# Kernel tuning notes

Hardware: AMD Instinct MI355X
Metric: run time of the kernel (lower is better)

## Reference

```python
import jax, jax.numpy as jnp
import numpy as np

HIDDEN = 2048
NUM_HEADS = 16
NUM_KV_HEADS = 4
HEAD_DIM = 128
ROPE_BASE = 10000.0


def apply_rope(x):
    # x: [B, H, S, D]; standard half-split RoPE
    B, H, S, D = x.shape
    half = D // 2
    inv_freq = 1.0 / (ROPE_BASE ** (jnp.arange(half, dtype=jnp.float32) / half))
    ang = jnp.arange(S, dtype=jnp.float32)[:, None] * inv_freq[None, :]  # [S, half]
    cos = jnp.cos(ang).astype(x.dtype)
    sin = jnp.sin(ang).astype(x.dtype)
    x1, x2 = x[..., :half], x[..., half:]
    return jnp.concatenate([x1 * cos - x2 * sin, x1 * sin + x2 * cos], axis=-1)


def setup_inputs() -> dict:
    key = jax.random.key(0)
    ks = jax.random.split(key, 6)
    B, S = 2, 2048
    sd = 1.0 / np.sqrt(HIDDEN)
    x = jax.random.normal(ks[0], (B, S, HIDDEN), dtype=jnp.float32)
    wq = jax.random.normal(ks[1], (NUM_HEADS * HEAD_DIM, HIDDEN), dtype=jnp.float32) * sd
    wk = jax.random.normal(ks[2], (NUM_KV_HEADS * HEAD_DIM, HIDDEN), dtype=jnp.float32) * sd
    wv = jax.random.normal(ks[3], (NUM_KV_HEADS * HEAD_DIM, HIDDEN), dtype=jnp.float32) * sd
    wo = jax.random.normal(ks[4], (HIDDEN, NUM_HEADS * HEAD_DIM), dtype=jnp.float32) * sd
    key_weights = jnp.ones((NUM_HEADS,), dtype=jnp.float32)
    return {"x": x, "wq": wq, "wk": wk, "wv": wv, "wo": wo, "key_weights": key_weights}


def reference(x, wq, wk, wv, wo, key_weights):
    B, S, _ = x.shape
    g = NUM_HEADS // NUM_KV_HEADS
    scale = HEAD_DIM ** -0.5
    # projections -> [B, H, S, D]
    q = (x @ wq.T).reshape(B, S, NUM_HEADS, HEAD_DIM).transpose(0, 2, 1, 3)
    k = (x @ wk.T).reshape(B, S, NUM_KV_HEADS, HEAD_DIM).transpose(0, 2, 1, 3)
    v = (x @ wv.T).reshape(B, S, NUM_KV_HEADS, HEAD_DIM).transpose(0, 2, 1, 3)
    q = apply_rope(q)
    k = apply_rope(k)
    # GQA expansion (repeat_interleave over head dim)
    k = jnp.repeat(k, g, axis=1)
    v = jnp.repeat(v, g, axis=1)
    # per-head key scaling fused into K
    k = k * key_weights[None, :, None, None]
    scores = jnp.einsum("bhqd,bhkd->bhqk", q, k) * scale
    causal = jnp.triu(jnp.ones((S, S), dtype=bool), k=1)
    scores = jnp.where(causal, -jnp.inf, scores)
    attn = jax.nn.softmax(scores, axis=-1)
    out = jnp.einsum("bhqk,bhkd->bhqd", attn, v)
    out = out.transpose(0, 2, 1, 3).reshape(B, S, NUM_HEADS * HEAD_DIM)
    return out @ wo.T
```

## Files before the change

kernel.cpp:

```cpp
#include <hip/hip_runtime.h>

#define S_LEN 2048
#define HID 2048
#define NH 16
#define HD 128
#define QKV_N 3072
#define KCOL 2048
#define VCOL 2560

typedef unsigned short ushort_t;
using bf16x8 = __attribute__((ext_vector_type(8))) __bf16;
using f32x4 = __attribute__((ext_vector_type(4))) float;
using ushort8 = __attribute__((ext_vector_type(8))) unsigned short;
using ushort4v = __attribute__((ext_vector_type(4))) unsigned short;

__device__ __forceinline__ unsigned short f2bf(float f) {
  unsigned int u = __float_as_uint(f);
  unsigned int r = u + 0x7FFFu + ((u >> 16) & 1u);
  return (unsigned short)(r >> 16);
}
__device__ __forceinline__ float bf2f(unsigned short h) {
  return __uint_as_float(((unsigned int)h) << 16);
}

__device__ __forceinline__ void gload_lds16(const ushort_t* g, ushort_t* lds) {
  __builtin_amdgcn_global_load_lds(
      (const __attribute__((address_space(1))) unsigned int*)g,
      (__attribute__((address_space(3))) unsigned int*)lds, 16, 0, 0);
}

__global__ void cast_bf16_kernel(const float* __restrict__ in, ushort_t* __restrict__ out, int n4) {
  int i = blockIdx.x * 256 + threadIdx.x;
  if (i >= n4) return;
  float4 v = reinterpret_cast<const float4*>(in)[i];
  ushort4v o;
  o.x = f2bf(v.x); o.y = f2bf(v.y); o.z = f2bf(v.z); o.w = f2bf(v.w);
  reinterpret_cast<ushort4v*>(out)[i] = o;
}

__global__ void rope_table_kernel(float* __restrict__ cosT, float* __restrict__ sinT) {
  int i = blockIdx.x * 256 + threadIdx.x;
  if (i >= S_LEN * 64) return;
  int s = i >> 6, j = i & 63;
  float inv = __expf(-(float)j * (9.210340371976184f / 64.0f));
  float ang = (float)s * inv;
  float sv, cv;
  sincosf(ang, &sv, &cv);
  cosT[i] = cv;
  sinT[i] = sv;
}

__global__ void rope_apply_kernel(ushort_t* __restrict__ base, const float* __restrict__ cosT,
                                  const float* __restrict__ sinT, const float* __restrict__ kw,
                                  int stride, int lognh, float scale, int useKw, int n) {
  int idx = blockIdx.x * 256 + threadIdx.x;
  if (idx >= n) return;
  int row = idx >> lognh;
  int p = idx & ((1 << lognh) - 1);
  int h = p >> 6, j = p & 63;
  int s = row & (S_LEN - 1);
  float c = cosT[(s << 6) + j];
  float sn = sinT[(s << 6) + j];
  long a = (long)row * stride + h * HD;
  float x1 = bf2f(base[a + j]);
  float x2 = bf2f(base[a + j + 64]);
  float wsc = useKw ? (scale * kw[h]) : scale;
  base[a + j] = f2bf((x1 * c - x2 * sn) * wsc);
  base[a + j + 64] = f2bf((x1 * sn + x2 * c) * wsc);
}

__global__ __launch_bounds__(256) void transpose_v_kernel(const ushort_t* __restrict__ qkv,
                                                          ushort_t* __restrict__ vt) {
  __shared__ ushort_t T[64][76];
  int bid = blockIdx.x;
  int dd = bid & 7;
  int tt = bid >> 3;
  int tid = threadIdx.x;
#pragma unroll
  for (int it = 0; it < 2; ++it) {
    int c = tid + it * 256;
    int i = c >> 3, j8 = c & 7;
    ushort8 v = *reinterpret_cast<const ushort8*>(
        qkv + (long)(tt * 64 + i) * QKV_N + VCOL + dd * 64 + j8 * 8);
    *reinterpret_cast<ushort8*>(&T[i][j8 * 8]) = v;
  }
  __syncthreads();
#pragma unroll
  for (int it = 0; it < 2; ++it) {
    int c = tid + it * 256;
    int jd = c >> 3, sc = c & 7;
    ushort8 o;
#pragma unroll
    for (int e = 0; e < 8; ++e) o[e] = T[sc * 8 + e][jd];
    int token = tt * 64 + sc * 8;
    int b = token >> 11, s = token & (S_LEN - 1);
    int vd = dd * 64 + jd;
    *reinterpret_cast<ushort8*>(vt + ((long)(b * 512 + vd) << 11) + s) = o;
  }
}

__device__ __forceinline__ void store_c(ushort_t* p, float v) { *p = f2bf(v); }
__device__ __forceinline__ void store_c(float* p, float v) { *p = v; }

template <typename OT>
__global__ __launch_bounds__(256) void gemm_bt_kernel(const ushort_t* __restrict__ A,
                                                      const ushort_t* __restrict__ W,
                                                      OT* __restrict__ C, int M, int N, int K) {
  __shared__ ushort_t As[128 * 32];
  __shared__ ushort_t Bs[128 * 32];
  const int tid = threadIdx.x;
  const int l = tid & 63, w = tid >> 6;
  const int wr = w >> 1, wc = w & 1;
  const int r = l & 15, g = l >> 4;
  const long arow0 = (long)blockIdx.y * 128;
  const long brow0 = (long)blockIdx.x * 128;

  f32x4 acc[4][4] = {};

  const int c0 = tid, c1 = tid + 256;
  const ushort_t* a_src0 = A + (arow0 + (c0 >> 2)) * K + ((c0 & 3) << 3);
  const ushort_t* a_src1 = A + (arow0 + (c1 >> 2)) * K + ((c1 & 3) << 3);
  const ushort_t* b_src0 = W + (brow0 + (c0 >> 2)) * K + ((c0 & 3) << 3);
  const ushort_t* b_src1 = W + (brow0 + (c1 >> 2)) * K + ((c1 & 3) << 3);
  ushort_t* a_dst0 = &As[c0 * 8];
  ushort_t* a_dst1 = &As[c1 * 8];
  ushort_t* b_dst0 = &Bs[c0 * 8];
  ushort_t* b_dst1 = &Bs[c1 * 8];

  for (int kk = 0; kk < K; kk += 32) {
    gload_lds16(a_src0 + kk, a_dst0);
    gload_lds16(a_src1 + kk, a_dst1);
    gload_lds16(b_src0 + kk, b_dst0);
    gload_lds16(b_src1 + kk, b_dst1);
    __syncthreads();
    bf16x8 af[4], bw[4];
#pragma unroll
    for (int mi = 0; mi < 4; ++mi)
      af[mi] = *reinterpret_cast<const bf16x8*>(&As[(wr * 64 + mi * 16 + r) * 32 + g * 8]);
#pragma unroll
    for (int ni = 0; ni < 4; ++ni)
      bw[ni] = *reinterpret_cast<const bf16x8*>(&Bs[(wc * 64 + ni * 16 + r) * 32 + g * 8]);
#pragma unroll
    for (int mi = 0; mi < 4; ++mi)
#pragma unroll
      for (int ni = 0; ni < 4; ++ni)
        acc[mi][ni] = __builtin_amdgcn_mfma_f32_16x16x32_bf16(af[mi], bw[ni], acc[mi][ni], 0, 0, 0);
    __syncthreads();
  }

#pragma unroll
  for (int mi = 0; mi < 4; ++mi)
#pragma unroll
    for (int ni = 0; ni < 4; ++ni) {
      int col = (int)brow0 + wc * 64 + ni * 16 + r;
#pragma unroll
      for (int j = 0; j < 4; ++j) {
        int row = (int)arow0 + wr * 64 + mi * 16 + g * 4 + j;
        store_c(&C[(long)row * N + col], acc[mi][ni][j]);
      }
    }
}

__global__ __launch_bounds__(256) void flash_attn_kernel(const ushort_t* __restrict__ qkv,
                                                         const ushort_t* __restrict__ Vt,
                                                         ushort_t* __restrict__ AO) {
  __shared__ ushort_t Ks[64 * 128];
  __shared__ ushort_t Vts[128 * 64];
  __shared__ ushort_t Ps[4][16 * 68];

  const int bid = blockIdx.x;
  const int pr = bid & 15;
  const int h = (bid >> 4) & 15;
  const int b = bid >> 8;
  const int tid = threadIdx.x;
  const int l = tid & 63, w = tid >> 6;
  const int r = l & 15, g = l >> 4;
  const int kvh = h >> 2;

  const ushort_t* Qb = qkv + (long)b * S_LEN * QKV_N + h * HD;
  const ushort_t* Kb = qkv + (long)b * S_LEN * QKV_N + KCOL + kvh * HD;
  const ushort_t* Vb = Vt + ((long)(b * 512 + kvh * HD) << 11);

  for (int pi = 0; pi < 2; ++pi) {
    const int qt = pi ? (31 - pr) : pr;
    const int qg = qt * 64 + w * 16;
    const long qrow0 = (long)b * S_LEN + qg;

    bf16x8 qa[4];
#pragma unroll
    for (int ks = 0; ks < 4; ++ks)
      qa[ks] = *reinterpret_cast<const bf16x8*>(Qb + (long)(qg + r) * QKV_N + ks * 32 + g * 8);

    f32x4 acc[8] = {};
    float mrow[4], lrow[4];
#pragma unroll
    for (int j = 0; j < 4; ++j) { mrow[j] = -1e30f; lrow[j] = 0.f; }

    for (int kv = 0; kv <= qt; ++kv) {
      __syncthreads();
#pragma unroll
      for (int i = 0; i < 4; ++i) {
        int c = tid + i * 256;
        int krow = c >> 4, cc = c & 15;
        int scc = cc ^ (krow & 7);
        gload_lds16(Kb + (long)(kv * 64 + krow) * QKV_N + scc * 8, &Ks[c * 8]);
      }
#pragma unroll
      for (int i = 0; i < 4; ++i) {
        int c = tid + i * 256;
        int vrow = c >> 3, cc = c & 7;
        int scc = cc ^ (vrow & 7);
        gload_lds16(Vb + ((long)vrow << 11) + kv * 64 + scc * 8, &Vts[c * 8]);
      }
      __syncthreads();

      f32x4 s[4] = {};
#pragma unroll
      for (int ks = 0; ks < 4; ++ks) {
        bf16x8 kf[4];
#pragma unroll
        for (int ni = 0; ni < 4; ++ni) {
          int n = ni * 16 + r;
          int chunk = (ks * 4 + g) ^ (n & 7);
          kf[ni] = *reinterpret_cast<const bf16x8*>(
              reinterpret_cast<const char*>(Ks) + n * 256 + chunk * 16);
        }
#pragma unroll
        for (int ni = 0; ni < 4; ++ni)
          s[ni] = __builtin_amdgcn_mfma_f32_16x16x32_bf16(qa[ks], kf[ni], s[ni], 0, 0, 0);
      }
      if (kv == qt) {
#pragma unroll
        for (int ni = 0; ni < 4; ++ni) {
          int key = kv * 64 + ni * 16 + r;
#pragma unroll
          for (int j = 0; j < 4; ++j) {
            int rowq = qg + g * 4 + j;
            if (key > rowq) s[ni][j] = -1e30f;
          }
        }
      }
#pragma unroll
      for (int j = 0; j < 4; ++j) {
        float mx = fmaxf(fmaxf(s[0][j], s[1][j]), fmaxf(s[2][j], s[3][j]));
        mx = fmaxf(mx, __shfl_xor(mx, 1));
        mx = fmaxf(mx, __shfl_xor(mx, 2));
        mx = fmaxf(mx, __shfl_xor(mx, 4));
        mx = fmaxf(mx, __shfl_xor(mx, 8));
        float mo = mrow[j];
        float mn = fmaxf(mo, mx);
        float ef = __expf(mo - mn);
        mrow[j] = mn;
        float psum = 0.f;
#pragma unroll
        for (int ni = 0; ni < 4; ++ni) {
          float p = __expf(s[ni][j] - mn);
          s[ni][j] = p;
          psum += p;
        }
        lrow[j] = lrow[j] * ef + psum;
#pragma unroll
        for (int ni = 0; ni < 8; ++ni) acc[ni][j] *= ef;
      }
#pragma unroll
      for (int ni = 0; ni < 4; ++ni)
#pragma unroll
        for (int j = 0; j < 4; ++j)
          Ps[w][(g * 4 + j) * 68 + ni * 16 + r] = f2bf(s[ni][j]);
#pragma unroll
      for (int ks2 = 0; ks2 < 2; ++ks2) {
        bf16x8 pa = *reinterpret_cast<const bf16x8*>(&Ps[w][r * 68 + ks2 * 32 + g * 8]);
#pragma unroll
        for (int ni = 0; ni < 8; ++ni) {
          int d = ni * 16 + r;
          int chunk = (ks2 * 4 + g) ^ (d & 7);
          bf16x8 vf = *reinterpret_cast<const bf16x8*>(
              reinterpret_cast<const char*>(Vts) + d * 128 + chunk * 16);
          acc[ni] = __builtin_amdgcn_mfma_f32_16x16x32_bf16(pa, vf, acc[ni], 0, 0, 0);
        }
      }
    }

#pragma unroll
    for (int j = 0; j < 4; ++j) {
      float lt = lrow[j];
      lt += __shfl_xor(lt, 1);
      lt += __shfl_xor(lt, 2);
      lt += __shfl_xor(lt, 4);
      lt += __shfl_xor(lt, 8);
      float inv = 1.0f / lt;
#pragma unroll
      for (int ni = 0; ni < 8; ++ni) acc[ni][j] *= inv;
    }
#pragma unroll
    for (int ni = 0; ni < 8; ++ni) {
      int col = h * HD + ni * 16 + r;
#pragma unroll
      for (int j = 0; j < 4; ++j) {
        long row = qrow0 + g * 4 + j;
        AO[row * HID + col] = f2bf(acc[ni][j]);
      }
    }
    __syncthreads();
  }
}

extern "C" void kernel_launch(void* const* d_in, const int* in_sizes, int n_in,
                              void* d_out, int out_size, void* d_ws, size_t ws_size,
                              hipStream_t stream) {
  const float* x = (const float*)d_in[0];
  const float* wq = (const float*)d_in[1];
  const float* wk = (const float*)d_in[2];
  const float* wv = (const float*)d_in[3];
  const float* wo = (const float*)d_in[4];
  const float* kw = (const float*)d_in[5];
  float* out = (float*)d_out;

  ushort_t* ws = (ushort_t*)d_ws;
  ushort_t* xb = ws;
  ushort_t* qkv = xb + 8388608;
  ushort_t* vt = qkv + 12582912;
  ushort_t* wqkv = vt + 2097152;
  float* cosT = (float*)(wqkv + 6291456);
  float* sinT = cosT + S_LEN * 64;

  cast_bf16_kernel<<<8192, 256, 0, stream>>>(x, xb, 2097152);
  cast_bf16_kernel<<<4096, 256, 0, stream>>>(wq, wqkv, 1048576);
  cast_bf16_kernel<<<1024, 256, 0, stream>>>(wk, wqkv + 2048 * 2048, 262144);
  cast_bf16_kernel<<<1024, 256, 0, stream>>>(wv, wqkv + 2560 * 2048, 262144);
  rope_table_kernel<<<512, 256, 0, stream>>>(cosT, sinT);

  gemm_bt_kernel<ushort_t><<<dim3(24, 32), 256, 0, stream>>>(xb, wqkv, qkv, 4096, QKV_N, 2048);

  rope_apply_kernel<<<16384, 256, 0, stream>>>(qkv, cosT, sinT, kw, QKV_N, 10,
                                               0.08838834764831845f, 1, 4194304);
  rope_apply_kernel<<<4096, 256, 0, stream>>>(qkv + KCOL, cosT, sinT, kw, QKV_N, 8,
                                              1.0f, 0, 1048576);

  transpose_v_kernel<<<512, 256, 0, stream>>>(qkv, vt);

  ushort_t* wob = wqkv;
  cast_bf16_kernel<<<4096, 256, 0, stream>>>(wo, wob, 1048576);

  flash_attn_kernel<<<512, 256, 0, stream>>>(qkv, vt, xb);

  gemm_bt_kernel<float><<<dim3(16, 32), 256, 0, stream>>>(xb, wob, out, 4096, 2048, 2048);
}
```

Baseline: 349.4 us.

## Fuse cast and RoPE launches; drop LDS staging in flash attention

Merges the four fp32-to-bf16 casts into one launch, and replaces the RoPE table plus two apply kernels with a single vectorized kernel that computes sin/cos inline. The flash attention kernel no longer stages K and V tiles in LDS. Each wave reads its MFMA fragments straight from global memory, and the kernel adds launch bounds for two blocks per SM, a remapped block order, and s_setprio around the MFMA sections. It also skips the softmax rescale when the running max grows by no more than 8 (lazy rescaling) and truncates P to bf16 instead of rounding it. The aim is to cut launch overhead and LDS and barrier cost, at the risk of redundant uncoalesced global loads that depend on L2 hits, plus a small precision change.

```diff
diff --git a/kernel.cpp b/kernel.cpp
--- a/kernel.cpp
+++ b/kernel.cpp
@@ -29,6 +29,23 @@
       (__attribute__((address_space(3))) unsigned int*)lds, 16, 0, 0);
 }
 
+__global__ void cast_fused_kernel(const float* __restrict__ x, const float* __restrict__ wq,
+                                  const float* __restrict__ wk, const float* __restrict__ wv,
+                                  ushort_t* __restrict__ xb, ushort_t* __restrict__ wqkv) {
+  int i = blockIdx.x * 256 + threadIdx.x;
+  const float* src;
+  ushort_t* dst;
+  int li;
+  if (i < 2097152) { src = x; dst = xb; li = i; }
+  else if (i < 3145728) { src = wq; dst = wqkv; li = i - 2097152; }
+  else if (i < 3407872) { src = wk; dst = wqkv + 4194304; li = i - 3145728; }
+  else { src = wv; dst = wqkv + 5242880; li = i - 3407872; }
+  float4 v = reinterpret_cast<const float4*>(src)[li];
+  ushort4v o;
+  o.x = f2bf(v.x); o.y = f2bf(v.y); o.z = f2bf(v.z); o.w = f2bf(v.w);
+  reinterpret_cast<ushort4v*>(dst)[li] = o;
+}
+
 __global__ void cast_bf16_kernel(const float* __restrict__ in, ushort_t* __restrict__ out, int n4) {
   int i = blockIdx.x * 256 + threadIdx.x;
   if (i >= n4) return;
@@ -38,35 +55,44 @@
   reinterpret_cast<ushort4v*>(out)[i] = o;
 }
 
-__global__ void rope_table_kernel(float* __restrict__ cosT, float* __restrict__ sinT) {
-  int i = blockIdx.x * 256 + threadIdx.x;
-  if (i >= S_LEN * 64) return;
-  int s = i >> 6, j = i & 63;
-  float inv = __expf(-(float)j * (9.210340371976184f / 64.0f));
-  float ang = (float)s * inv;
-  float sv, cv;
-  sincosf(ang, &sv, &cv);
-  cosT[i] = cv;
-  sinT[i] = sv;
-}
-
-__global__ void rope_apply_kernel(ushort_t* __restrict__ base, const float* __restrict__ cosT,
-                                  const float* __restrict__ sinT, const float* __restrict__ kw,
-                                  int stride, int lognh, float scale, int useKw, int n) {
+__global__ void rope_fused_kernel(ushort_t* __restrict__ qkv, const float* __restrict__ kw) {
   int idx = blockIdx.x * 256 + threadIdx.x;
-  if (idx >= n) return;
-  int row = idx >> lognh;
-  int p = idx & ((1 << lognh) - 1);
-  int h = p >> 6, j = p & 63;
+  int row, colbase, j0;
+  float wsc;
+  if (idx < 524288) {
+    row = idx >> 7;
+    int p = idx & 127;
+    int h = p >> 3;
+    j0 = (p & 7) * 8;
+    colbase = h * HD;
+    wsc = 0.08838834764831845f * kw[h];
+  } else {
+    int t = idx - 524288;
+    row = t >> 5;
+    int p = t & 31;
+    int h = p >> 3;
+    j0 = (p & 7) * 8;
+    colbase = KCOL + h * HD;
+    wsc = 1.0f;
+  }
   int s = row & (S_LEN - 1);
-  float c = cosT[(s << 6) + j];
-  float sn = sinT[(s << 6) + j];
-  long a = (long)row * stride + h * HD;
-  float x1 = bf2f(base[a + j]);
-  float x2 = bf2f(base[a + j + 64]);
-  float wsc = useKw ? (scale * kw[h]) : scale;
-  base[a + j] = f2bf((x1 * c - x2 * sn) * wsc);
-  base[a + j + 64] = f2bf((x1 * sn + x2 * c) * wsc);
+  long base = (long)row * QKV_N + colbase;
+  ushort8 x1 = *reinterpret_cast<const ushort8*>(qkv + base + j0);
+  ushort8 x2 = *reinterpret_cast<const ushort8*>(qkv + base + j0 + 64);
+  ushort8 o1, o2;
+#pragma unroll
+  for (int e = 0; e < 8; ++e) {
+    int j = j0 + e;
+    float inv = __expf(-(float)j * (9.210340371976184f / 64.0f));
+    float ang = (float)s * inv;
+    float sv, cv;
+    sincosf(ang, &sv, &cv);
+    float a = bf2f(x1[e]), bb = bf2f(x2[e]);
+    o1[e] = f2bf((a * cv - bb * sv) * wsc);
+    o2[e] = f2bf((a * sv + bb * cv) * wsc);
+  }
+  *reinterpret_cast<ushort8*>(qkv + base + j0) = o1;
+  *reinterpret_cast<ushort8*>(qkv + base + j0 + 64) = o2;
 }
 
 __global__ __launch_bounds__(256) void transpose_v_kernel(const ushort_t* __restrict__ qkv,
@@ -161,17 +187,17 @@
     }
 }
 
-__global__ __launch_bounds__(256) void flash_attn_kernel(const ushort_t* __restrict__ qkv,
-                                                         const ushort_t* __restrict__ Vt,
-                                                         ushort_t* __restrict__ AO) {
-  __shared__ ushort_t Ks[64 * 128];
-  __shared__ ushort_t Vts[128 * 64];
-  __shared__ ushort_t Ps[4][16 * 68];
-
-  const int bid = blockIdx.x;
-  const int pr = bid & 15;
-  const int h = (bid >> 4) & 15;
-  const int b = bid >> 8;
+__global__ __launch_bounds__(256, 2) void flash_attn_kernel(const ushort_t* __restrict__ qkv,
+                                                            const ushort_t* __restrict__ Vt,
+                                                            ushort_t* __restrict__ AO) {
+  __shared__ ushort_t Ps[4][16 * 64];
+
+  const int bid0 = blockIdx.x;
+  const int o = (bid0 & 7) * 64 + (bid0 >> 3);
+  const int pr = o & 15;
+  const int hb = o >> 4;
+  const int h = hb >> 1;
+  const int b = hb & 1;
   const int tid = threadIdx.x;
   const int l = tid & 63, w = tid >> 6;
   const int r = l & 15, g = l >> 4;
@@ -197,38 +223,23 @@
     for (int j = 0; j < 4; ++j) { mrow[j] = -1e30f; lrow[j] = 0.f; }
 
     for (int kv = 0; kv <= qt; ++kv) {
-      __syncthreads();
-#pragma unroll
-      for (int i = 0; i < 4; ++i) {
-        int c = tid + i * 256;
-        int krow = c >> 4, cc = c & 15;
-        int scc = cc ^ (krow & 7);
-        gload_lds16(Kb + (long)(kv * 64 + krow) * QKV_N + scc * 8, &Ks[c * 8]);
-      }
-#pragma unroll
-      for (int i = 0; i < 4; ++i) {
-        int c = tid + i * 256;
-        int vrow = c >> 3, cc = c & 7;
-        int scc = cc ^ (vrow & 7);
-        gload_lds16(Vb + ((long)vrow << 11) + kv * 64 + scc * 8, &Vts[c * 8]);
-      }
-      __syncthreads();
+      const ushort_t* Kt0 = Kb + (long)(kv * 64) * QKV_N;
 
       f32x4 s[4] = {};
+      __builtin_amdgcn_s_setprio(1);
 #pragma unroll
       for (int ks = 0; ks < 4; ++ks) {
         bf16x8 kf[4];
 #pragma unroll
-        for (int ni = 0; ni < 4; ++ni) {
-          int n = ni * 16 + r;
-          int chunk = (ks * 4 + g) ^ (n & 7);
+        for (int ni = 0; ni < 4; ++ni)
           kf[ni] = *reinterpret_cast<const bf16x8*>(
-              reinterpret_cast<const char*>(Ks) + n * 256 + chunk * 16);
-        }
+              Kt0 + (long)(ni * 16 + r) * QKV_N + ks * 32 + g * 8);
 #pragma unroll
         for (int ni = 0; ni < 4; ++ni)
           s[ni] = __builtin_amdgcn_mfma_f32_16x16x32_bf16(qa[ks], kf[ni], s[ni], 0, 0, 0);
       }
+      __builtin_amdgcn_s_setprio(0);
+
       if (kv == qt) {
 #pragma unroll
         for (int ni = 0; ni < 4; ++ni) {
@@ -240,45 +251,65 @@
           }
         }
       }
+
+      float mx[4];
+      float dm = -1e30f;
 #pragma unroll
       for (int j = 0; j < 4; ++j) {
-        float mx = fmaxf(fmaxf(s[0][j], s[1][j]), fmaxf(s[2][j], s[3][j]));
-        mx = fmaxf(mx, __shfl_xor(mx, 1));
-        mx = fmaxf(mx, __shfl_xor(mx, 2));
-        mx = fmaxf(mx, __shfl_xor(mx, 4));
-        mx = fmaxf(mx, __shfl_xor(mx, 8));
-        float mo = mrow[j];
-        float mn = fmaxf(mo, mx);
-        float ef = __expf(mo - mn);
-        mrow[j] = mn;
-        float psum = 0.f;
+        float m3 = fmaxf(fmaxf(s[0][j], s[1][j]), fmaxf(s[2][j], s[3][j]));
+        m3 = fmaxf(m3, __shfl_xor(m3, 1));
+        m3 = fmaxf(m3, __shfl_xor(m3, 2));
+        m3 = fmaxf(m3, __shfl_xor(m3, 4));
+        m3 = fmaxf(m3, __shfl_xor(m3, 8));
+        mx[j] = m3;
+        dm = fmaxf(dm, m3 - mrow[j]);
+      }
+      if (!__all(dm <= 8.0f)) {
+#pragma unroll
+        for (int j = 0; j < 4; ++j) {
+          float mn = fmaxf(mrow[j], mx[j]);
+          float ef = __expf(mrow[j] - mn);
+          mrow[j] = mn;
+          lrow[j] *= ef;
+#pragma unroll
+          for (int ni = 0; ni < 8; ++ni) acc[ni][j] *= ef;
+        }
+      }
+#pragma unroll
+      for (int j = 0; j < 4; ++j) {
+        float ps = 0.f;
 #pragma unroll
         for (int ni = 0; ni < 4; ++ni) {
-          float p = __expf(s[ni][j] - mn);
+          float p = __expf(s[ni][j] - mrow[j]);
           s[ni][j] = p;
-          psum += p;
-        }
-        lrow[j] = lrow[j] * ef + psum;
-#pragma unroll
-        for (int ni = 0; ni < 8; ++ni) acc[ni][j] *= ef;
-      }
+          ps += p;
+        }
+        lrow[j] += ps;
+      }
+
 #pragma unroll
       for (int ni = 0; ni < 4; ++ni)
 #pragma unroll
-        for (int j = 0; j < 4; ++j)
-          Ps[w][(g * 4 + j) * 68 + ni * 16 + r] = f2bf(s[ni][j]);
-#pragma unroll
-      for (int ks2 = 0; ks2 < 2; ++ks2) {
-        bf16x8 pa = *reinterpret_cast<const bf16x8*>(&Ps[w][r * 68 + ks2 * 32 + g * 8]);
+        for (int j = 0; j < 4; ++j) {
+          int row = g * 4 + j;
+          int chunk = (ni * 2 + (r >> 3)) ^ (row & 7);
+          Ps[w][row * 64 + chunk * 8 + (r & 7)] =
+              (ushort_t)(__float_as_uint(s[ni][j]) >> 16);
+        }
+      bf16x8 pa[2];
+      pa[0] = *reinterpret_cast<const bf16x8*>(&Ps[w][r * 64 + (((g) ^ (r & 7)) << 3)]);
+      pa[1] = *reinterpret_cast<const bf16x8*>(&Ps[w][r * 64 + (((4 + g) ^ (r & 7)) << 3)]);
+
+      __builtin_amdgcn_s_setprio(1);
+#pragma unroll
+      for (int ks2 = 0; ks2 < 2; ++ks2)
 #pragma unroll
         for (int ni = 0; ni < 8; ++ni) {
-          int d = ni * 16 + r;
-          int chunk = (ks2 * 4 + g) ^ (d & 7);
           bf16x8 vf = *reinterpret_cast<const bf16x8*>(
-              reinterpret_cast<const char*>(Vts) + d * 128 + chunk * 16);
-          acc[ni] = __builtin_amdgcn_mfma_f32_16x16x32_bf16(pa, vf, acc[ni], 0, 0, 0);
-        }
-      }
+              Vb + ((long)(ni * 16 + r) << 11) + kv * 64 + ks2 * 32 + g * 8);
+          acc[ni] = __builtin_amdgcn_mfma_f32_16x16x32_bf16(pa[ks2], vf, acc[ni], 0, 0, 0);
+        }
+      __builtin_amdgcn_s_setprio(0);
     }
 
 #pragma unroll
@@ -301,7 +332,6 @@
         AO[row * HID + col] = f2bf(acc[ni][j]);
       }
     }
-    __syncthreads();
   }
 }
 
@@ -321,21 +351,12 @@
   ushort_t* qkv = xb + 8388608;
   ushort_t* vt = qkv + 12582912;
   ushort_t* wqkv = vt + 2097152;
-  float* cosT = (float*)(wqkv + 6291456);
-  float* sinT = cosT + S_LEN * 64;
-
-  cast_bf16_kernel<<<8192, 256, 0, stream>>>(x, xb, 2097152);
-  cast_bf16_kernel<<<4096, 256, 0, stream>>>(wq, wqkv, 1048576);
-  cast_bf16_kernel<<<1024, 256, 0, stream>>>(wk, wqkv + 2048 * 2048, 262144);
-  cast_bf16_kernel<<<1024, 256, 0, stream>>>(wv, wqkv + 2560 * 2048, 262144);
-  rope_table_kernel<<<512, 256, 0, stream>>>(cosT, sinT);
+
+  cast_fused_kernel<<<14336, 256, 0, stream>>>(x, wq, wk, wv, xb, wqkv);
 
   gemm_bt_kernel<ushort_t><<<dim3(24, 32), 256, 0, stream>>>(xb, wqkv, qkv, 4096, QKV_N, 2048);
 
-  rope_apply_kernel<<<16384, 256, 0, stream>>>(qkv, cosT, sinT, kw, QKV_N, 10,
-                                               0.08838834764831845f, 1, 4194304);
-  rope_apply_kernel<<<4096, 256, 0, stream>>>(qkv + KCOL, cosT, sinT, kw, QKV_N, 8,
-                                              1.0f, 0, 1048576);
+  rope_fused_kernel<<<2560, 256, 0, stream>>>(qkv, kw);
 
   transpose_v_kernel<<<512, 256, 0, stream>>>(qkv, vt);
 
```

Measured after the change: 494.3 us. 41.4% more time.
